# Kernel tuning notes

Hardware: AMD Instinct MI355X
Metric: run time of the kernel (lower is better)

The kernel has to match this reference:

```python
import jax, jax.numpy as jnp
import numpy as np


def _fft_feats(x):
    # x: [B, 3, H, W] float32
    B, C, H, W = x.shape
    gray = 0.299 * x[:, 0] + 0.587 * x[:, 1] + 0.114 * x[:, 2]  # [B,H,W]
    mag = jnp.abs(jnp.fft.fftshift(jnp.fft.fft2(gray), axes=(-2, -1))) + 1e-8
    mag = mag / (mag.max(axis=(-2, -1), keepdims=True) + 1e-8)
    m = mag.reshape(B, -1)
    n = m.shape[1]
    mean = m.mean(axis=1)
    std = jnp.clip(jnp.std(m, axis=1, ddof=1), 1e-8, None)  # torch unbiased std
    mx = m.max(axis=1)
    mn = m.min(axis=1)
    gt_mean = (m > mean[:, None]).astype(jnp.float32).mean(axis=1)
    # torch.median returns the lower of the two middle values for even n
    med = jnp.sort(m, axis=1)[:, (n - 1) // 2]
    q1 = mag[:, : H // 4].mean(axis=(1, 2))
    q2 = mag[:, H // 4 : H // 2].mean(axis=(1, 2))
    q3 = mag[:, H // 2 : 3 * H // 4].mean(axis=(1, 2))
    q4 = mag[:, 3 * H // 4 :].mean(axis=(1, 2))
    gt_half = (m > 0.5).astype(jnp.float32).mean(axis=1)
    gt_tenth = (m > 0.1).astype(jnp.float32).mean(axis=1)
    feats = jnp.stack([mean, std, mx, mn, gt_mean, med, q1, q2, q3, q4, gt_half, gt_tenth], axis=1)
    return jnp.clip(feats, -10.0, 10.0)  # [B,12]


def _bn(h, gamma, beta):
    # BatchNorm1d, training-mode forward (batch statistics, biased var), eps=1e-5
    mu = h.mean(axis=0)
    var = h.var(axis=0)
    return gamma * (h - mu) / jnp.sqrt(var + 1e-5) + beta


def _mlp(f, W1, b1, g1, be1, W2, b2, g2, be2, W3, b3):
    h = jax.nn.relu(_bn(f @ W1 + b1, g1, be1))  # Dropout(0.1) treated as identity (eval)
    h = jax.nn.relu(_bn(h @ W2 + b2, g2, be2))
    return h @ W3 + b3


def setup_inputs() -> dict:
    key = jax.random.key(0)
    ks = jax.random.split(key, 8)
    B, H, W = 64, 512, 512
    D = 512  # output_dim
    x = jax.random.normal(ks[0], (B, 3, H, W), dtype=jnp.float32)
    W1 = jax.random.normal(ks[1], (12, 64), dtype=jnp.float32) * 0.2
    b1 = jnp.zeros((64,), jnp.float32)
    g1 = jnp.ones((64,), jnp.float32)
    be1 = jnp.zeros((64,), jnp.float32)
    W2 = jax.random.normal(ks[2], (64, 128), dtype=jnp.float32) * 0.1
    b2 = jnp.zeros((128,), jnp.float32)
    g2 = jnp.ones((128,), jnp.float32)
    be2 = jnp.zeros((128,), jnp.float32)
    W3 = jax.random.normal(ks[3], (128, D), dtype=jnp.float32) * 0.08
    b3 = jnp.zeros((D,), jnp.float32)
    return {"x": x, "W1": W1, "b1": b1, "g1": g1, "be1": be1,
            "W2": W2, "b2": b2, "g2": g2, "be2": be2, "W3": W3, "b3": b3}


def reference(x, W1, b1, g1, be1, W2, b2, g2, be2, W3, b3):
    feats = _fft_feats(x)
    return _mlp(feats, W1, b1, g1, be1, W2, b2, g2, be2, W3, b3)
```

## Files before the change

kernel.cpp:

```cpp
#include <hip/hip_runtime.h>
#include <math.h>

#ifndef M_PI
#define M_PI 3.14159265358979323846
#endif

#define BB 64
#define HH 512
#define WW 512
#define NPIX (HH*WW)
#define MED_K 131072u
#define WS 260
#define PADI(i) ((i) + ((i) >> 5))

__device__ __forceinline__ float2 cmulf(float2 a, float2 b){
  return make_float2(a.x*b.x - a.y*b.y, a.x*b.y + a.y*b.x);
}
__device__ __forceinline__ unsigned rev9(unsigned v){ return __brev(v) >> 23; }

__device__ __forceinline__ double wred_add(double v){
  #pragma unroll
  for (int o = 32; o > 0; o >>= 1) v += __shfl_down(v, o, 64);
  return v;
}
__device__ __forceinline__ float wred_min(float v){
  #pragma unroll
  for (int o = 32; o > 0; o >>= 1) v = fminf(v, __shfl_down(v, o, 64));
  return v;
}
__device__ __forceinline__ float wred_max(float v){
  #pragma unroll
  for (int o = 32; o > 0; o >>= 1) v = fmaxf(v, __shfl_down(v, o, 64));
  return v;
}
__device__ __forceinline__ unsigned wred_addu(unsigned v){
  #pragma unroll
  for (int o = 32; o > 0; o >>= 1) v += __shfl_down(v, o, 64);
  return v;
}
__device__ __forceinline__ float wred_add_all(float v){
  #pragma unroll
  for (int o = 32; o > 0; o >>= 1) v += __shfl_xor(v, o, 64);
  return v;
}

__global__ __launch_bounds__(256) void row_fft_kernel(const float* __restrict__ x,
                                                      float2* __restrict__ out){
  __shared__ float sre[528], sim[528];
  __shared__ float2 tw[256];
  int t = threadIdx.x;
  {
    double a = -2.0 * M_PI * (double)t / 512.0;
    tw[t] = make_float2((float)cos(a), (float)sin(a));
  }
  int row = blockIdx.x;
  int b = row >> 9;
  const float* rp = x + (size_t)b*3*NPIX + (size_t)(row & 511)*WW;
  const float* gp = rp + NPIX;
  const float* bp = rp + 2*NPIX;
  for (int k = t; k < 512; k += 256){
    float g = 0.299f*rp[k] + 0.587f*gp[k] + 0.114f*bp[k];
    int ri = (int)rev9((unsigned)k);
    sre[PADI(ri)] = g; sim[PADI(ri)] = 0.f;
  }
  __syncthreads();
  #pragma unroll
  for (int st = 1; st <= 9; ++st){
    int half = 1 << (st-1);
    int k = t & (half - 1);
    int i1 = ((t >> (st-1)) << st) + k;
    int i2 = i1 + half;
    int p1 = PADI(i1), p2 = PADI(i2);
    float2 w = tw[k << (9 - st)];
    float2 u = make_float2(sre[p1], sim[p1]);
    float2 raw = make_float2(sre[p2], sim[p2]);
    float2 v = cmulf(w, raw);
    sre[p1] = u.x + v.x; sim[p1] = u.y + v.y;
    sre[p2] = u.x - v.x; sim[p2] = u.y - v.y;
    __syncthreads();
  }
  float2* o = out + (size_t)row*WW;
  for (int k = t; k < 512; k += 256)
    if (k <= 256){ int p = PADI(k); o[k] = make_float2(sre[p], sim[p]); }
}

__global__ __launch_bounds__(512) void col_fft_kernel(const float2* __restrict__ in,
    float* __restrict__ magc,
    unsigned* __restrict__ dmax, unsigned* __restrict__ dmin,
    double* __restrict__ sum, double* __restrict__ sumsq, double* __restrict__ qsum,
    unsigned* __restrict__ hist1)
{
  __shared__ float2 s[512*16];
  __shared__ float2 tw[256];
  __shared__ unsigned h[2048];
  __shared__ double bufd[6][8];
  __shared__ float buff[2][8];
  int t = threadIdx.x;
  if (t < 256){
    double a = -2.0 * M_PI * (double)t / 512.0;
    tw[t] = make_float2((float)cos(a), (float)sin(a));
  }
  for (int i = t; i < 2048; i += 512) h[i] = 0;
  int b = blockIdx.x / 17;
  int j0 = (blockIdx.x % 17) << 4;
  const float2* base = in + (size_t)b*NPIX;
  for (int idx = t; idx < 512*16; idx += 512){
    int e = idx >> 4, c = idx & 15;
    int j = j0 + c;
    float2 v = (j <= 256) ? base[(size_t)e*WW + j] : make_float2(0.f, 0.f);
    s[(int)rev9((unsigned)e)*16 + c] = v;
  }
  __syncthreads();
  #pragma unroll
  for (int st = 1; st <= 9; ++st){
    int half = 1 << (st-1);
    #pragma unroll
    for (int qq = 0; qq < 8; ++qq){
      int tt = t + (qq << 9);
      int c = tt & 15;
      int kk = tt >> 4;
      int k = kk & (half - 1);
      int i1 = ((kk >> (st-1)) << st) + k;
      int i2 = i1 + half;
      float2 w = tw[k << (9 - st)];
      float2 u = s[i1*16 + c];
      float2 v = cmulf(w, s[i2*16 + c]);
      s[i1*16 + c] = make_float2(u.x + v.x, u.y + v.y);
      s[i2*16 + c] = make_float2(u.x - v.x, u.y - v.y);
    }
    __syncthreads();
  }
  double lsum=0.0, lsq=0.0, lq0=0.0, lq1=0.0, lq2=0.0, lq3=0.0;
  float lmn = 3.4e38f, lmx = 0.f;
  float* mo = magc + (size_t)b*(512*WS);
  for (int idx = t; idx < 512*16; idx += 512){
    int e = idx >> 4, c = idx & 15;
    int j = j0 + c;
    if (j > 256) continue;
    float2 v = s[e*16 + c];
    float m = sqrtf(v.x*v.x + v.y*v.y) + 1e-8f;
    int si = (e + 256) & 511;
    mo[(size_t)si*WS + j] = m;
    unsigned w = (j == 0 || j == 256) ? 1u : 2u;
    double md = (double)m;
    double wm = (w == 2u) ? md + md : md;
    lsum += wm;
    lsq  += wm * md;
    lmn = fminf(lmn, m); lmx = fmaxf(lmx, m);
    atomicAdd(&h[__float_as_uint(m) >> 20], w);
    int qa = si >> 7;
    lq0 += (qa==0)?md:0.0; lq1 += (qa==1)?md:0.0; lq2 += (qa==2)?md:0.0; lq3 += (qa==3)?md:0.0;
    if (w == 2u){
      int qb = ((512 - si) & 511) >> 7;
      lq0 += (qb==0)?md:0.0; lq1 += (qb==1)?md:0.0; lq2 += (qb==2)?md:0.0; lq3 += (qb==3)?md:0.0;
    }
  }
  int lane = t & 63, wv = t >> 6;
  double r0 = wred_add(lsum), r1 = wred_add(lsq);
  double r2 = wred_add(lq0), r3 = wred_add(lq1), r4 = wred_add(lq2), r5 = wred_add(lq3);
  float fmn = wred_min(lmn), fmx = wred_max(lmx);
  if (lane == 0){
    bufd[0][wv]=r0; bufd[1][wv]=r1; bufd[2][wv]=r2;
    bufd[3][wv]=r3; bufd[4][wv]=r4; bufd[5][wv]=r5;
    buff[0][wv]=fmn; buff[1][wv]=fmx;
  }
  __syncthreads();
  if (t == 0){
    double s0=0,s1=0,s2=0,s3=0,s4=0,s5=0; float mn=3.4e38f, mx=0.f;
    for (int i = 0; i < 8; ++i){
      s0+=bufd[0][i]; s1+=bufd[1][i]; s2+=bufd[2][i];
      s3+=bufd[3][i]; s4+=bufd[4][i]; s5+=bufd[5][i];
      mn=fminf(mn,buff[0][i]); mx=fmaxf(mx,buff[1][i]);
    }
    atomicAdd(sum + b, s0);
    atomicAdd(sumsq + b, s1);
    atomicAdd(qsum + b*4 + 0, s2);
    atomicAdd(qsum + b*4 + 1, s3);
    atomicAdd(qsum + b*4 + 2, s4);
    atomicAdd(qsum + b*4 + 3, s5);
    atomicMin(dmin + b, __float_as_uint(mn));
    atomicMax(dmax + b, __float_as_uint(mx));
  }
  unsigned* hb = hist1 + (size_t)b*2048;
  for (int i = t; i < 2048; i += 512){
    unsigned c = h[i];
    if (c) atomicAdd(&hb[i], c);
  }
}

__global__ void scan1_kernel(const unsigned* __restrict__ hist,
                             unsigned* __restrict__ sel, unsigned* __restrict__ rem){
  int b = blockIdx.x;
  const unsigned* hb = hist + (size_t)b*2048;
  __shared__ unsigned part[256];
  int t = threadIdx.x;
  unsigned s = 0;
  for (int i = 0; i < 8; ++i) s += hb[t*8 + i];
  part[t] = s; __syncthreads();
  if (t == 0){
    unsigned target = MED_K, cum = 0; int seg = 0;
    for (; seg < 256; ++seg){ if (cum + part[seg] >= target) break; cum += part[seg]; }
    unsigned r = target - cum;
    int bin = seg*8;
    for (;; ++bin){ unsigned c = hb[bin]; if (c >= r) break; r -= c; }
    sel[b] = (unsigned)bin;
    rem[b] = r;
  }
}

__global__ __launch_bounds__(256) void pass2_kernel(const float4* __restrict__ magc4,
    const unsigned* __restrict__ sel1, const double* __restrict__ sum,
    const unsigned* __restrict__ dmax,
    unsigned* __restrict__ hist2, unsigned* __restrict__ cnt_gtm,
    unsigned* __restrict__ cnt_half, unsigned* __restrict__ cnt_tenth)
{
  __shared__ unsigned h[16384];
  __shared__ unsigned rb[3][8];
  int t = threadIdx.x, b = blockIdx.x;
  for (int i = t; i < 16384; i += 256) h[i] = 0;
  __syncthreads();
  unsigned s1 = sel1[b];
  float meanf = (float)(sum[b] / (double)NPIX);
  float d = __uint_as_float(dmax[b]) + 1e-8f;
  float th = 0.5f*d, tl = 0.1f*d;
  const float4* p = magc4 + (size_t)b*(512*(WS/4)) + (size_t)blockIdx.y*128*(WS/4);
  unsigned lgm = 0, lh = 0, lt = 0;
  for (int idx = t; idx < 128*(WS/4); idx += 256){
    float4 v = p[idx];
    int k = idx % (WS/4);
    int jc0 = k*4;
    float a[4] = {v.x, v.y, v.z, v.w};
    #pragma unroll
    for (int q = 0; q < 4; ++q){
      int jc = jc0 + q;
      if (jc > 256) continue;
      unsigned w = (jc == 0 || jc == 256) ? 1u : 2u;
      float m = a[q];
      unsigned bits = __float_as_uint(m);
      if ((bits >> 20) == s1) atomicAdd(&h[(bits >> 6) & 0x3fffu], w);
      lgm += (m > meanf) ? w : 0u;
      lh  += (m > th) ? w : 0u;
      lt  += (m > tl) ? w : 0u;
    }
  }
  int lane = t & 63, wv = t >> 6;
  unsigned g0 = wred_addu(lgm), g1 = wred_addu(lh), g2 = wred_addu(lt);
  if (lane == 0){ rb[0][wv]=g0; rb[1][wv]=g1; rb[2][wv]=g2; }
  __syncthreads();
  if (t == 0){
    unsigned a0=0,a1=0,a2=0;
    for (int i = 0; i < 4; ++i){ a0+=rb[0][i]; a1+=rb[1][i]; a2+=rb[2][i]; }
    atomicAdd(cnt_gtm + b, a0);
    atomicAdd(cnt_half + b, a1);
    atomicAdd(cnt_tenth + b, a2);
  }
  unsigned* hb = hist2 + (size_t)b*16384;
  for (int i = t; i < 16384; i += 256){
    unsigned c = h[i];
    if (c) atomicAdd(&hb[i], c);
  }
}

__global__ void scan2_kernel(const unsigned* __restrict__ hist,
    const unsigned* __restrict__ sel1, const unsigned* __restrict__ rem1,
    unsigned* __restrict__ medbits){
  int b = blockIdx.x;
  const unsigned* hb = hist + (size_t)b*16384;
  __shared__ unsigned part[256];
  int t = threadIdx.x;
  unsigned s = 0;
  for (int i = 0; i < 64; ++i) s += hb[t*64 + i];
  part[t] = s; __syncthreads();
  if (t == 0){
    unsigned target = rem1[b], cum = 0; int seg = 0;
    for (; seg < 256; ++seg){ if (cum + part[seg] >= target) break; cum += part[seg]; }
    unsigned r = target - cum;
    int bin = seg*64;
    for (;; ++bin){ unsigned c = hb[bin]; if (c >= r) break; r -= c; }
    medbits[b] = (sel1[b] << 20) | ((unsigned)bin << 6) | 32u;
  }
}

__global__ void feats_kernel(const unsigned* __restrict__ dmax, const unsigned* __restrict__ dmin,
    const double* __restrict__ sum, const double* __restrict__ sumsq, const double* __restrict__ qsum,
    const unsigned* __restrict__ cnt_half, const unsigned* __restrict__ cnt_tenth,
    const unsigned* __restrict__ cnt_gtmean, const unsigned* __restrict__ medbits,
    float* __restrict__ feats)
{
  int b = threadIdx.x;
  if (b >= BB) return;
  float maxv = __uint_as_float(dmax[b]);
  float d = maxv + 1e-8f;
  double dd = (double)d;
  double n = (double)NPIX;
  double sm = sum[b] / dd;
  double sq = sumsq[b] / (dd*dd);
  double mean = sm / n;
  double var = (sq - sm*sm/n) / (n - 1.0);
  if (var < 0.0) var = 0.0;
  float stdv = (float)sqrt(var);
  if (stdv < 1e-8f) stdv = 1e-8f;
  float mx = maxv / d;
  float mn = __uint_as_float(dmin[b]) / d;
  float gtm = (float)((double)cnt_gtmean[b] / n);
  float med = __uint_as_float(medbits[b]) / d;
  float q0 = (float)(qsum[b*4+0] / dd * (1.0/65536.0));
  float q1 = (float)(qsum[b*4+1] / dd * (1.0/65536.0));
  float q2 = (float)(qsum[b*4+2] / dd * (1.0/65536.0));
  float q3 = (float)(qsum[b*4+3] / dd * (1.0/65536.0));
  float gh = (float)((double)cnt_half[b] / n);
  float gt = (float)((double)cnt_tenth[b] / n);
  float f[12] = {(float)mean, stdv, mx, mn, gtm, med, q0, q1, q2, q3, gh, gt};
  #pragma unroll
  for (int i = 0; i < 12; ++i){
    float v = f[i];
    v = fminf(fmaxf(v, -10.f), 10.f);
    feats[b*12 + i] = v;
  }
}

__global__ __launch_bounds__(64) void mlp1_kernel(const float* __restrict__ feats,
    const float* __restrict__ W1, const float* __restrict__ b1,
    const float* __restrict__ g1, const float* __restrict__ be1,
    float* __restrict__ h1t)
{
  int c = blockIdx.x, r = threadIdx.x;
  float acc = b1[c];
  #pragma unroll
  for (int k = 0; k < 12; ++k) acc += feats[r*12 + k] * W1[k*64 + c];
  float mu = wred_add_all(acc) * (1.f/BB);
  float dv = acc - mu;
  float var = wred_add_all(dv*dv) * (1.f/BB);
  float scv = g1[c] * __frsqrt_rn(var + 1e-5f);
  scv = g1[c] / sqrtf(var + 1e-5f);
  float v = dv*scv + be1[c];
  h1t[c*BB + r] = v > 0.f ? v : 0.f;
}

__global__ __launch_bounds__(64) void mlp2_kernel(const float* __restrict__ h1t,
    const float* __restrict__ W2, const float* __restrict__ b2,
    const float* __restrict__ g2, const float* __restrict__ be2,
    float* __restrict__ h2t)
{
  int c = blockIdx.x, r = threadIdx.x;
  float acc = b2[c];
  #pragma unroll 4
  for (int k = 0; k < 64; ++k) acc += h1t[k*BB + r] * W2[k*128 + c];
  float mu = wred_add_all(acc) * (1.f/BB);
  float dv = acc - mu;
  float var = wred_add_all(dv*dv) * (1.f/BB);
  float scv = g2[c] / sqrtf(var + 1e-5f);
  float v = dv*scv + be2[c];
  h2t[c*BB + r] = v > 0.f ? v : 0.f;
}

__global__ __launch_bounds__(256) void mlp3_kernel(const float* __restrict__ h2t,
    const float* __restrict__ W3, const float* __restrict__ b3,
    float* __restrict__ out)
{
  int r = threadIdx.x & 63;
  int w = threadIdx.x >> 6;
  int c = blockIdx.x*4 + w;
  float acc = b3[c];
  #pragma unroll 4
  for (int k = 0; k < 128; ++k) acc += h2t[k*BB + r] * W3[k*512 + c];
  out[r*512 + c] = acc;
}

extern "C" void kernel_launch(void* const* d_in, const int* in_sizes, int n_in,
                              void* d_out, int out_size, void* d_ws, size_t ws_size,
                              hipStream_t stream) {
  (void)in_sizes; (void)n_in; (void)out_size; (void)ws_size;
  const float* x   = (const float*)d_in[0];
  const float* W1  = (const float*)d_in[1];
  const float* b1  = (const float*)d_in[2];
  const float* g1  = (const float*)d_in[3];
  const float* be1 = (const float*)d_in[4];
  const float* W2  = (const float*)d_in[5];
  const float* b2  = (const float*)d_in[6];
  const float* g2  = (const float*)d_in[7];
  const float* be2 = (const float*)d_in[8];
  const float* W3  = (const float*)d_in[9];
  const float* b3  = (const float*)d_in[10];
  float* out = (float*)d_out;

  char* ws = (char*)d_ws;
  float2* bufc = (float2*)ws;
  float*  magc = (float*)(ws + 134217728);
  unsigned* hist1 = (unsigned*)(ws + 134217728 + 34078720);
  unsigned* hist2 = (unsigned*)(ws + 168296448 + 524288);
  char* sc = ws + 168820736 + 4194304;
  unsigned* dmax      = (unsigned*)(sc + 0);
  unsigned* dmin      = (unsigned*)(sc + 256);
  double*   sum       = (double*)(sc + 512);
  double*   sumsq     = (double*)(sc + 1024);
  double*   qsum      = (double*)(sc + 1536);
  unsigned* cnt_half  = (unsigned*)(sc + 3584);
  unsigned* cnt_tenth = (unsigned*)(sc + 3840);
  unsigned* cnt_gtm   = (unsigned*)(sc + 4096);
  unsigned* sel1      = (unsigned*)(sc + 4352);
  unsigned* rem1      = (unsigned*)(sc + 4608);
  unsigned* medbits   = (unsigned*)(sc + 4864);
  float*    feats     = (float*)(sc + 5120);
  float*    h1t       = (float*)(sc + 8192);
  float*    h2t       = (float*)(sc + 8192 + 16384);

  hipMemsetAsync(hist1, 0, 524288 + 4194304, stream);
  hipMemsetAsync(sc, 0, 8192, stream);
  hipMemsetAsync(dmin, 0xFF, 256, stream);

  row_fft_kernel<<<BB*HH, 256, 0, stream>>>(x, bufc);
  col_fft_kernel<<<BB*17, 512, 0, stream>>>(bufc, magc, dmax, dmin, sum, sumsq, qsum, hist1);
  scan1_kernel<<<BB, 256, 0, stream>>>(hist1, sel1, rem1);
  pass2_kernel<<<dim3(BB, 4), 256, 0, stream>>>((const float4*)magc, sel1, sum, dmax,
      hist2, cnt_gtm, cnt_half, cnt_tenth);
  scan2_kernel<<<BB, 256, 0, stream>>>(hist2, sel1, rem1, medbits);
  feats_kernel<<<1, 64, 0, stream>>>(dmax, dmin, sum, sumsq, qsum, cnt_half, cnt_tenth, cnt_gtm, medbits, feats);
  mlp1_kernel<<<64, 64, 0, stream>>>(feats, W1, b1, g1, be1, h1t);
  mlp2_kernel<<<128, 64, 0, stream>>>(h1t, W2, b2, g2, be2, h2t);
  mlp3_kernel<<<128, 256, 0, stream>>>(h2t, W3, b3, out);
}
```

Measured before the change: 470.4 us.

## Pack two real rows per complex FFT and precompute twiddles in global memory

The row FFT now places two real grayscale rows into the real and imaginary parts of one 512-point complex FFT. The two spectra are separated afterwards using Hermitian symmetry, which halves the number of row-FFT blocks and butterfly work. Input loads are vectorised to float4. Twiddle factors are computed once by a small init kernel instead of with double-precision cos/sin in every block. This adds an extra kernel launch and a small separation step, and mixes the two rows in float32 arithmetic, which could shift rounding slightly.

```diff
diff --git a/kernel.cpp b/kernel.cpp
--- a/kernel.cpp
+++ b/kernel.cpp
@@ -44,24 +44,37 @@
   return v;
 }
 
+__global__ void twiddle_init_kernel(float2* __restrict__ twg){
+  int t = threadIdx.x;
+  double a = -2.0 * M_PI * (double)t / 512.0;
+  twg[t] = make_float2((float)cos(a), (float)sin(a));
+}
+
 __global__ __launch_bounds__(256) void row_fft_kernel(const float* __restrict__ x,
+                                                      const float2* __restrict__ twg,
                                                       float2* __restrict__ out){
   __shared__ float sre[528], sim[528];
   __shared__ float2 tw[256];
   int t = threadIdx.x;
-  {
-    double a = -2.0 * M_PI * (double)t / 512.0;
-    tw[t] = make_float2((float)cos(a), (float)sin(a));
-  }
-  int row = blockIdx.x;
-  int b = row >> 9;
-  const float* rp = x + (size_t)b*3*NPIX + (size_t)(row & 511)*WW;
-  const float* gp = rp + NPIX;
-  const float* bp = rp + 2*NPIX;
-  for (int k = t; k < 512; k += 256){
-    float g = 0.299f*rp[k] + 0.587f*gp[k] + 0.114f*bp[k];
-    int ri = (int)rev9((unsigned)k);
-    sre[PADI(ri)] = g; sim[PADI(ri)] = 0.f;
+  tw[t] = twg[t];
+  int pair = blockIdx.x;
+  int b = pair >> 8, hp = pair & 255;
+  const float* base = x + (size_t)b*3*NPIX + (size_t)(2*hp)*WW;
+  int rsel = t >> 7;
+  int f4i = t & 127;
+  const float* rowbase = base + rsel*WW;
+  float4 rv = ((const float4*)rowbase)[f4i];
+  float4 gv = ((const float4*)(rowbase + NPIX))[f4i];
+  float4 bv = ((const float4*)(rowbase + 2*NPIX))[f4i];
+  float g[4] = {0.299f*rv.x + 0.587f*gv.x + 0.114f*bv.x,
+                0.299f*rv.y + 0.587f*gv.y + 0.114f*bv.y,
+                0.299f*rv.z + 0.587f*gv.z + 0.114f*bv.z,
+                0.299f*rv.w + 0.587f*gv.w + 0.114f*bv.w};
+  int col0 = f4i << 2;
+  #pragma unroll
+  for (int q = 0; q < 4; ++q){
+    int p = PADI((int)rev9((unsigned)(col0 + q)));
+    if (rsel == 0) sre[p] = g[q]; else sim[p] = g[q];
   }
   __syncthreads();
   #pragma unroll
@@ -79,12 +92,24 @@
     sre[p2] = u.x - v.x; sim[p2] = u.y - v.y;
     __syncthreads();
   }
-  float2* o = out + (size_t)row*WW;
-  for (int k = t; k < 512; k += 256)
-    if (k <= 256){ int p = PADI(k); o[k] = make_float2(sre[p], sim[p]); }
+  int row0 = (b << 9) + 2*hp;
+  float2* o0 = out + (size_t)row0*WW;
+  float2* o1 = o0 + WW;
+  #pragma unroll
+  for (int kk = 0; kk < 2; ++kk){
+    int k = t + (kk << 8);
+    if (k > 256) continue;
+    int mk = (512 - k) & 511;
+    int pk = PADI(k), pmk = PADI(mk);
+    float zr = sre[pk], zi = sim[pk];
+    float wr = sre[pmk], wi = sim[pmk];
+    o0[k] = make_float2(0.5f*(zr + wr), 0.5f*(zi - wi));
+    o1[k] = make_float2(0.5f*(zi + wi), 0.5f*(wr - zr));
+  }
 }
 
 __global__ __launch_bounds__(512) void col_fft_kernel(const float2* __restrict__ in,
+    const float2* __restrict__ twg,
     float* __restrict__ magc,
     unsigned* __restrict__ dmax, unsigned* __restrict__ dmin,
     double* __restrict__ sum, double* __restrict__ sumsq, double* __restrict__ qsum,
@@ -96,10 +121,7 @@
   __shared__ double bufd[6][8];
   __shared__ float buff[2][8];
   int t = threadIdx.x;
-  if (t < 256){
-    double a = -2.0 * M_PI * (double)t / 512.0;
-    tw[t] = make_float2((float)cos(a), (float)sin(a));
-  }
+  if (t < 256) tw[t] = twg[t];
   for (int i = t; i < 2048; i += 512) h[i] = 0;
   int b = blockIdx.x / 17;
   int j0 = (blockIdx.x % 17) << 4;
@@ -331,8 +353,7 @@
   float mu = wred_add_all(acc) * (1.f/BB);
   float dv = acc - mu;
   float var = wred_add_all(dv*dv) * (1.f/BB);
-  float scv = g1[c] * __frsqrt_rn(var + 1e-5f);
-  scv = g1[c] / sqrtf(var + 1e-5f);
+  float scv = g1[c] / sqrtf(var + 1e-5f);
   float v = dv*scv + be1[c];
   h1t[c*BB + r] = v > 0.f ? v : 0.f;
 }
@@ -404,13 +425,15 @@
   float*    feats     = (float*)(sc + 5120);
   float*    h1t       = (float*)(sc + 8192);
   float*    h2t       = (float*)(sc + 8192 + 16384);
+  float2*   twg       = (float2*)(sc + 8192 + 16384 + 32768);
 
   hipMemsetAsync(hist1, 0, 524288 + 4194304, stream);
   hipMemsetAsync(sc, 0, 8192, stream);
   hipMemsetAsync(dmin, 0xFF, 256, stream);
 
-  row_fft_kernel<<<BB*HH, 256, 0, stream>>>(x, bufc);
-  col_fft_kernel<<<BB*17, 512, 0, stream>>>(bufc, magc, dmax, dmin, sum, sumsq, qsum, hist1);
+  twiddle_init_kernel<<<1, 256, 0, stream>>>(twg);
+  row_fft_kernel<<<BB*256, 256, 0, stream>>>(x, twg, bufc);
+  col_fft_kernel<<<BB*17, 512, 0, stream>>>(bufc, twg, magc, dmax, dmin, sum, sumsq, qsum, hist1);
   scan1_kernel<<<BB, 256, 0, stream>>>(hist1, sel1, rem1);
   pass2_kernel<<<dim3(BB, 4), 256, 0, stream>>>((const float4*)magc, sel1, sum, dmax,
       hist2, cnt_gtm, cnt_half, cnt_tenth);
```

Result: no change. 469.3 us (-0.2%).
